# Kernel tuning notes

Measured on AMD Instinct MI355X. Metric: run time of the kernel, lower is better.

The kernel has to match this reference:

```python
import jax, jax.numpy as jnp
import numpy as np

B, S, D = 4, 2048, 768
H, DH = 12, 64  # num heads, head dim


def setup_inputs() -> dict:
    key = jax.random.key(0)
    ks = jax.random.split(key, 4)
    scale = 0.02
    return {
        "hidden_states": jax.random.normal(ks[0], (B, S, D), dtype=jnp.float32),
        "attention_mask": jnp.zeros((B, 1, 1, S), dtype=jnp.float32),
        "Wq": jax.random.normal(ks[1], (D, D), dtype=jnp.float32) * scale,
        "bq": jnp.zeros((D,), dtype=jnp.float32),
        "Wk": jax.random.normal(ks[2], (D, D), dtype=jnp.float32) * scale,
        "bk": jnp.zeros((D,), dtype=jnp.float32),
        "Wv": jax.random.normal(ks[3], (D, D), dtype=jnp.float32) * scale,
        "bv": jnp.zeros((D,), dtype=jnp.float32),
    }


def _split_heads(x):
    # [B, S, D] -> [B, H, S, DH]
    b, s, _ = x.shape
    return x.reshape(b, s, H, DH).transpose(0, 2, 1, 3)


def reference(hidden_states, attention_mask, Wq, bq, Wk, bk, Wv, bv):
    q = _split_heads(hidden_states @ Wq.T + bq)
    k = _split_heads(hidden_states @ Wk.T + bk)
    v = _split_heads(hidden_states @ Wv.T + bv)
    # scores: [B, H, S, S]
    scores = jnp.einsum("bhqd,bhkd->bhqk", q, k) / jnp.sqrt(jnp.float32(DH))
    scores = scores + attention_mask
    probs = jax.nn.softmax(scores, axis=-1)
    # dropout prob = 0.0 (eval) -> identity
    ctx = jnp.einsum("bhqk,bhkd->bhqd", probs, v)
    ctx = ctx.transpose(0, 2, 1, 3).reshape(hidden_states.shape[0], hidden_states.shape[1], D)
    return ctx
```

## Files before the change

kernel.cpp:

```cpp
#include <hip/hip_runtime.h>

#define S_LEN 2048
#define DMODEL 768
#define NH 12
#define DHEAD 64
#define BATCH 4
#define MROWS (BATCH * S_LEN)
#define NQKV 2304

using short8 = __attribute__((ext_vector_type(8))) short;
using f32x4  = __attribute__((ext_vector_type(4))) float;

typedef const __attribute__((address_space(1))) void* gas_ptr;
typedef __attribute__((address_space(3))) void* las_ptr;

__device__ __forceinline__ void gl2lds16(const void* g, void* l) {
  __builtin_amdgcn_global_load_lds((gas_ptr)(unsigned long long)g,
                                   (las_ptr)(unsigned int)(unsigned long long)l,
                                   16, 0, 0);
}

__device__ inline unsigned short f2bf(float f) {
  union { float f; unsigned int u; } c; c.f = f;
  unsigned int u = c.u;
  unsigned int r = (u + 0x7FFFu + ((u >> 16) & 1u)) >> 16;
  return (unsigned short)r;
}

__device__ inline unsigned int pack2bf(float a, float b) {
  union { float f; unsigned int u; } ca, cb;
  ca.f = a; cb.f = b;
  unsigned int ua = ca.u, ub = cb.u;
  ua = (ua + 0x7FFFu + ((ua >> 16) & 1u)) >> 16;
  ub = (ub + 0x7FFFu + ((ub >> 16) & 1u)) & 0xFFFF0000u;
  return ua | ub;
}

__global__ __launch_bounds__(256) void prep_kernel(
    const float* __restrict__ hs, const float* __restrict__ Wq,
    const float* __restrict__ Wk, const float* __restrict__ Wv,
    const float* __restrict__ mask,
    unsigned short* __restrict__ Xb, unsigned short* __restrict__ Wall,
    float* __restrict__ mask2)
{
  const int NX = MROWS * DMODEL / 4;
  const int NW = DMODEL * DMODEL / 4;
  const int NM = (BATCH * S_LEN) / 4;
  int i = blockIdx.x * 256 + threadIdx.x;
  if (i < NX) {
    float4 f = ((const float4*)hs)[i];
    ushort4 o = { f2bf(f.x), f2bf(f.y), f2bf(f.z), f2bf(f.w) };
    ((ushort4*)Xb)[i] = o;
  } else if (i < NX + 3 * NW) {
    int j = i - NX;
    int sec = j / NW, r = j - sec * NW;
    const float* src = (sec == 0) ? Wq : (sec == 1) ? Wk : Wv;
    float4 f = ((const float4*)src)[r];
    ushort4 o = { f2bf(f.x), f2bf(f.y), f2bf(f.z), f2bf(f.w) };
    ((ushort4*)(Wall + (size_t)sec * DMODEL * DMODEL))[r] = o;
  } else if (i < NX + 3 * NW + NM) {
    int r = i - NX - 3 * NW;
    float4 m = ((const float4*)mask)[r];
    float4 o = { m.x - 10.f, m.y - 10.f, m.z - 10.f, m.w - 10.f };
    ((float4*)mask2)[r] = o;
  }
}

__global__ __launch_bounds__(256) void qkv_gemm(
    const unsigned short* __restrict__ Xb,
    const unsigned short* __restrict__ Wall,
    const float* __restrict__ bq,
    const float* __restrict__ bk,
    const float* __restrict__ bv,
    unsigned short* __restrict__ Out)
{
  __shared__ __align__(16) short As[128][64];
  __shared__ __align__(16) short Bs[128][64];

  int m0 = blockIdx.y * 128;
  int n0 = blockIdx.x * 128;
  int t = threadIdx.x;
  int w = t >> 6, lane = t & 63, lg = lane >> 4, lc = lane & 15;
  int wr = (w >> 1) * 64, wc = (w & 1) * 64;

  int srow = lane >> 3;
  int schunk = (lane & 7) ^ srow;

  f32x4 acc[4][4] = {};

  for (int k0 = 0; k0 < DMODEL; k0 += 64) {
    __syncthreads();
    for (int it = 0; it < 4; ++it) {
      int rb = w * 32 + it * 8;
      int r = rb + srow;
      gl2lds16(&Xb[(size_t)(m0 + r) * DMODEL + k0 + schunk * 8], &As[rb][0]);
      gl2lds16(&Wall[(size_t)(n0 + r) * DMODEL + k0 + schunk * 8], &Bs[rb][0]);
    }
    __syncthreads();
    for (int ks = 0; ks < 2; ++ks) {
      short8 a[4], b[4];
      for (int mt = 0; mt < 4; ++mt)
        a[mt] = *(const short8*)&As[wr + mt * 16 + lc][(((ks * 4 + lg) ^ (lc & 7))) * 8];
      for (int nt = 0; nt < 4; ++nt)
        b[nt] = *(const short8*)&Bs[wc + nt * 16 + lc][(((ks * 4 + lg) ^ (lc & 7))) * 8];
      for (int mt = 0; mt < 4; ++mt)
        for (int nt = 0; nt < 4; ++nt)
          acc[mt][nt] = __builtin_amdgcn_mfma_f32_16x16x32_bf16(a[mt], b[nt], acc[mt][nt], 0, 0, 0);
    }
  }

  for (int mt = 0; mt < 4; ++mt) {
    int row = m0 + wr + mt * 16 + lg * 4;
    for (int nt = 0; nt < 4; ++nt) {
      int col = n0 + wc + nt * 16 + lc;
      float bb = (col < 768) ? bq[col] : (col < 1536) ? bk[col - 768] : bv[col - 1536];
      float sc = (col < 768) ? 0.125f : 1.0f;
      for (int i = 0; i < 4; ++i)
        Out[(size_t)(row + i) * NQKV + col] = f2bf((acc[mt][nt][i] + bb) * sc);
    }
  }
}

__global__ __launch_bounds__(256) void v_transpose(
    const unsigned short* __restrict__ QKV,
    unsigned short* __restrict__ Vt)
{
  int st = blockIdx.x, h = blockIdx.y, b = blockIdx.z;
  __shared__ __align__(16) short Ls[64][72];
  int t = threadIdx.x;
  int s0 = st * 64;
  int lr = t >> 3, ls = (t & 7) * 8;
  for (int it = 0; it < 2; ++it) {
    int r = lr + it * 32;
    *(int4*)&Ls[r][ls] =
        *(const int4*)&QKV[(size_t)(b * S_LEN + s0 + r) * NQKV + 1536 + h * DHEAD + ls];
  }
  __syncthreads();
  int d = t & 63, sq = t >> 6;
  size_t obase = ((size_t)((b * NH + h) * DHEAD + d)) * S_LEN + s0;
  for (int it = 0; it < 2; ++it) {
    int ss = sq + it * 4;
    short8 vv;
    for (int j = 0; j < 8; ++j) vv[j] = Ls[ss * 8 + j][d];
    *(short8*)&Vt[obase + ss * 8] = vv;
  }
}

__global__ __launch_bounds__(256, 6) void flash_attn(
    const unsigned short* __restrict__ QKV,
    const unsigned short* __restrict__ Vt,
    const float* __restrict__ mask2,
    float* __restrict__ out)
{
  int qt = blockIdx.x, h = blockIdx.y, b = blockIdx.z;
  __shared__ __align__(16) short Ks[64][64];
  __shared__ __align__(16) short Vts[64][64];
  __shared__ __align__(16) short Ps[4][16][72];

  int t = threadIdx.x, w = t >> 6, lane = t & 63, lg = lane >> 4, lc = lane & 15;
  int q0 = qt * 64;
  int srow = lane >> 3;
  int schunk = (lane & 7) ^ srow;

  short8 qf[2];
  {
    size_t qrow = (size_t)(b * S_LEN + q0 + w * 16 + lc) * NQKV + h * DHEAD;
    qf[0] = *(const short8*)&QKV[qrow + lg * 8];
    qf[1] = *(const short8*)&QKV[qrow + 32 + lg * 8];
  }

  f32x4 psv = {0.f, 0.f, 0.f, 0.f};
  f32x4 o[4] = {};
  size_t vtbase = (size_t)((b * NH + h) * DHEAD) * S_LEN;
  const float* mrow = mask2 + (size_t)b * S_LEN;

  for (int kt = 0; kt < S_LEN / 64; ++kt) {
    int k0 = kt * 64;
    __syncthreads();
    {
      size_t kbase = (size_t)(b * S_LEN + k0) * NQKV + 768 + h * DHEAD;
      for (int it = 0; it < 2; ++it) {
        int rb = w * 16 + it * 8;
        int r = rb + srow;
        gl2lds16(&QKV[kbase + (size_t)r * NQKV + schunk * 8], &Ks[rb][0]);
        gl2lds16(&Vt[vtbase + (size_t)r * S_LEN + k0 + schunk * 8], &Vts[rb][0]);
      }
    }
    __syncthreads();

    f32x4 s[4] = {};
    for (int kk = 0; kk < 2; ++kk)
      for (int mt = 0; mt < 4; ++mt) {
        short8 ak = *(const short8*)&Ks[mt * 16 + lc][((kk * 4 + lg) ^ (lc & 7)) * 8];
        s[mt] = __builtin_amdgcn_mfma_f32_16x16x32_bf16(ak, qf[kk], s[mt], 0, 0, 0);
      }

    for (int mt = 0; mt < 4; ++mt) {
      float4 mv = *(const float4*)&mrow[k0 + mt * 16 + lg * 4];
      float p0 = __expf(s[mt][0] + mv.x);
      float p1 = __expf(s[mt][1] + mv.y);
      float p2 = __expf(s[mt][2] + mv.z);
      float p3 = __expf(s[mt][3] + mv.w);
      psv[0] += p0; psv[1] += p1; psv[2] += p2; psv[3] += p3;
      uint2 d;
      d.x = pack2bf(p0, p1);
      d.y = pack2bf(p2, p3);
      *(uint2*)&Ps[w][lc][mt * 16 + lg * 4] = d;
    }

    __builtin_amdgcn_s_waitcnt(0);

    for (int kk = 0; kk < 2; ++kk) {
      short8 ap = *(const short8*)&Ps[w][lc][kk * 32 + lg * 8];
      for (int nt = 0; nt < 4; ++nt) {
        short8 bv = *(const short8*)&Vts[nt * 16 + lc][((kk * 4 + lg) ^ (lc & 7)) * 8];
        o[nt] = __builtin_amdgcn_mfma_f32_16x16x32_bf16(ap, bv, o[nt], 0, 0, 0);
      }
    }
  }

  float l = psv[0] + psv[1] + psv[2] + psv[3];
  l += __shfl_xor(l, 16, 64);
  l += __shfl_xor(l, 32, 64);
  float inv = 1.0f / l;
  float lv[4];
  for (int i = 0; i < 4; ++i) lv[i] = __shfl(inv, lg * 4 + i, 64);

  for (int nt = 0; nt < 4; ++nt)
    for (int i = 0; i < 4; ++i) {
      int q = q0 + w * 16 + lg * 4 + i;
      out[(size_t)(b * S_LEN + q) * DMODEL + h * DHEAD + nt * 16 + lc] = o[nt][i] * lv[i];
    }
}

extern "C" void kernel_launch(void* const* d_in, const int* in_sizes, int n_in,
                              void* d_out, int out_size, void* d_ws, size_t ws_size,
                              hipStream_t stream) {
  const float* hs   = (const float*)d_in[0];
  const float* mask = (const float*)d_in[1];
  const float* Wq   = (const float*)d_in[2];
  const float* bq   = (const float*)d_in[3];
  const float* Wk   = (const float*)d_in[4];
  const float* bk   = (const float*)d_in[5];
  const float* Wv   = (const float*)d_in[6];
  const float* bv   = (const float*)d_in[7];
  float* out = (float*)d_out;

  char* ws = (char*)d_ws;
  const size_t XB_BYTES   = (size_t)MROWS * DMODEL * 2;
  const size_t QKV_BYTES  = (size_t)MROWS * NQKV * 2;
  const size_t WALL_BYTES = (size_t)NQKV * DMODEL * 2;
  unsigned short* Xb    = (unsigned short*)ws;
  unsigned short* QKV   = (unsigned short*)(ws + XB_BYTES);
  unsigned short* Wall  = (unsigned short*)(ws + XB_BYTES + QKV_BYTES);
  float*          mask2 = (float*)(ws + XB_BYTES + QKV_BYTES + WALL_BYTES);
  unsigned short* Vtg   = Xb;

  const int NX = MROWS * DMODEL / 4;
  const int NW = DMODEL * DMODEL / 4;
  const int NM = (BATCH * S_LEN) / 4;
  int nprep = NX + 3 * NW + NM;
  prep_kernel<<<(nprep + 255) / 256, 256, 0, stream>>>(hs, Wq, Wk, Wv, mask, Xb, Wall, mask2);

  qkv_gemm<<<dim3(NQKV / 128, MROWS / 128), 256, 0, stream>>>(Xb, Wall, bq, bk, bv, QKV);

  v_transpose<<<dim3(S_LEN / 64, NH, BATCH), 256, 0, stream>>>(QKV, Vtg);

  flash_attn<<<dim3(S_LEN / 64, NH, BATCH), 256, 0, stream>>>(QKV, Vtg, mask2, out);
}
```

Measured before the change: 244.8 us.

## Switch flash attention to 32x32 MFMA with 128-row query tiles

The attention kernel now has each wave handle 32 query rows using 32x32x16 bf16 MFMA instead of 16x16x32, so each block covers 128 queries and the grid halves. Every K/V tile loaded into LDS is therefore reused across twice as many queries, which cuts global and LDS traffic per unit of work, and the larger MFMA shape needs fewer fragment loads. The cost is more registers per wave (launch bounds lowered to 4) and fewer blocks, which may reduce occupancy. The QKV GEMM epilogue loop order is also swapped so bias and scale are computed once per column.

```diff
diff --git a/kernel.cpp b/kernel.cpp
--- a/kernel.cpp
+++ b/kernel.cpp
@@ -10,6 +10,7 @@
 
 using short8 = __attribute__((ext_vector_type(8))) short;
 using f32x4  = __attribute__((ext_vector_type(4))) float;
+using f32x16 = __attribute__((ext_vector_type(16))) float;
 
 typedef const __attribute__((address_space(1))) void* gas_ptr;
 typedef __attribute__((address_space(3))) void* las_ptr;
@@ -109,12 +110,12 @@
     }
   }
 
-  for (int mt = 0; mt < 4; ++mt) {
-    int row = m0 + wr + mt * 16 + lg * 4;
-    for (int nt = 0; nt < 4; ++nt) {
-      int col = n0 + wc + nt * 16 + lc;
-      float bb = (col < 768) ? bq[col] : (col < 1536) ? bk[col - 768] : bv[col - 1536];
-      float sc = (col < 768) ? 0.125f : 1.0f;
+  for (int nt = 0; nt < 4; ++nt) {
+    int col = n0 + wc + nt * 16 + lc;
+    float bb = (col < 768) ? bq[col] : (col < 1536) ? bk[col - 768] : bv[col - 1536];
+    float sc = (col < 768) ? 0.125f : 1.0f;
+    for (int mt = 0; mt < 4; ++mt) {
+      int row = m0 + wr + mt * 16 + lg * 4;
       for (int i = 0; i < 4; ++i)
         Out[(size_t)(row + i) * NQKV + col] = f2bf((acc[mt][nt][i] + bb) * sc);
     }
@@ -146,7 +147,7 @@
   }
 }
 
-__global__ __launch_bounds__(256, 6) void flash_attn(
+__global__ __launch_bounds__(256, 4) void flash_attn(
     const unsigned short* __restrict__ QKV,
     const unsigned short* __restrict__ Vt,
     const float* __restrict__ mask2,
@@ -155,22 +156,23 @@
   int qt = blockIdx.x, h = blockIdx.y, b = blockIdx.z;
   __shared__ __align__(16) short Ks[64][64];
   __shared__ __align__(16) short Vts[64][64];
-  __shared__ __align__(16) short Ps[4][16][72];
-
-  int t = threadIdx.x, w = t >> 6, lane = t & 63, lg = lane >> 4, lc = lane & 15;
-  int q0 = qt * 64;
+  __shared__ __align__(16) short Ps[4][32][68];
+
+  int t = threadIdx.x, w = t >> 6, lane = t & 63;
+  int m31 = lane & 31, hf = lane >> 5;
+  int q0 = qt * 128;
   int srow = lane >> 3;
   int schunk = (lane & 7) ^ srow;
 
-  short8 qf[2];
+  short8 qf[4];
   {
-    size_t qrow = (size_t)(b * S_LEN + q0 + w * 16 + lc) * NQKV + h * DHEAD;
-    qf[0] = *(const short8*)&QKV[qrow + lg * 8];
-    qf[1] = *(const short8*)&QKV[qrow + 32 + lg * 8];
-  }
-
-  f32x4 psv = {0.f, 0.f, 0.f, 0.f};
-  f32x4 o[4] = {};
+    size_t qrow = (size_t)(b * S_LEN + q0 + w * 32 + m31) * NQKV + h * DHEAD;
+    for (int kk = 0; kk < 4; ++kk)
+      qf[kk] = *(const short8*)&QKV[qrow + kk * 16 + hf * 8];
+  }
+
+  float lsum = 0.f;
+  f32x16 o[2] = {};
   size_t vtbase = (size_t)((b * NH + h) * DHEAD) * S_LEN;
   const float* mrow = mask2 + (size_t)b * S_LEN;
 
@@ -188,48 +190,51 @@
     }
     __syncthreads();
 
-    f32x4 s[4] = {};
-    for (int kk = 0; kk < 2; ++kk)
-      for (int mt = 0; mt < 4; ++mt) {
-        short8 ak = *(const short8*)&Ks[mt * 16 + lc][((kk * 4 + lg) ^ (lc & 7)) * 8];
-        s[mt] = __builtin_amdgcn_mfma_f32_16x16x32_bf16(ak, qf[kk], s[mt], 0, 0, 0);
-      }
-
-    for (int mt = 0; mt < 4; ++mt) {
-      float4 mv = *(const float4*)&mrow[k0 + mt * 16 + lg * 4];
-      float p0 = __expf(s[mt][0] + mv.x);
-      float p1 = __expf(s[mt][1] + mv.y);
-      float p2 = __expf(s[mt][2] + mv.z);
-      float p3 = __expf(s[mt][3] + mv.w);
-      psv[0] += p0; psv[1] += p1; psv[2] += p2; psv[3] += p3;
-      uint2 d;
-      d.x = pack2bf(p0, p1);
-      d.y = pack2bf(p2, p3);
-      *(uint2*)&Ps[w][lc][mt * 16 + lg * 4] = d;
-    }
+    f32x16 s[2] = {};
+    for (int kk = 0; kk < 4; ++kk)
+      for (int mt = 0; mt < 2; ++mt) {
+        int r = mt * 32 + m31;
+        short8 ak = *(const short8*)&Ks[r][((kk * 2 + hf) ^ (r & 7)) * 8];
+        s[mt] = __builtin_amdgcn_mfma_f32_32x32x16_bf16(ak, qf[kk], s[mt], 0, 0, 0);
+      }
+
+    for (int mt = 0; mt < 2; ++mt)
+      for (int g = 0; g < 4; ++g) {
+        float4 mv = *(const float4*)&mrow[k0 + mt * 32 + g * 8 + hf * 4];
+        float p0 = __expf(s[mt][g * 4 + 0] + mv.x);
+        float p1 = __expf(s[mt][g * 4 + 1] + mv.y);
+        float p2 = __expf(s[mt][g * 4 + 2] + mv.z);
+        float p3 = __expf(s[mt][g * 4 + 3] + mv.w);
+        lsum += (p0 + p1) + (p2 + p3);
+        uint2 d2;
+        d2.x = pack2bf(p0, p1);
+        d2.y = pack2bf(p2, p3);
+        *(uint2*)&Ps[w][m31][mt * 32 + g * 8 + hf * 4] = d2;
+      }
 
     __builtin_amdgcn_s_waitcnt(0);
 
-    for (int kk = 0; kk < 2; ++kk) {
-      short8 ap = *(const short8*)&Ps[w][lc][kk * 32 + lg * 8];
-      for (int nt = 0; nt < 4; ++nt) {
-        short8 bv = *(const short8*)&Vts[nt * 16 + lc][((kk * 4 + lg) ^ (lc & 7)) * 8];
-        o[nt] = __builtin_amdgcn_mfma_f32_16x16x32_bf16(ap, bv, o[nt], 0, 0, 0);
-      }
-    }
-  }
-
-  float l = psv[0] + psv[1] + psv[2] + psv[3];
-  l += __shfl_xor(l, 16, 64);
-  l += __shfl_xor(l, 32, 64);
-  float inv = 1.0f / l;
-  float lv[4];
-  for (int i = 0; i < 4; ++i) lv[i] = __shfl(inv, lg * 4 + i, 64);
-
-  for (int nt = 0; nt < 4; ++nt)
-    for (int i = 0; i < 4; ++i) {
-      int q = q0 + w * 16 + lg * 4 + i;
-      out[(size_t)(b * S_LEN + q) * DMODEL + h * DHEAD + nt * 16 + lc] = o[nt][i] * lv[i];
+    for (int kk = 0; kk < 4; ++kk) {
+      short8 ap = *(const short8*)&Ps[w][m31][kk * 16 + hf * 8];
+      for (int nt = 0; nt < 2; ++nt) {
+        int r = nt * 32 + m31;
+        short8 bv = *(const short8*)&Vts[r][((kk * 2 + hf) ^ (r & 7)) * 8];
+        o[nt] = __builtin_amdgcn_mfma_f32_32x32x16_bf16(ap, bv, o[nt], 0, 0, 0);
+      }
+    }
+  }
+
+  lsum += __shfl_xor(lsum, 32, 64);
+  float inv = 1.0f / lsum;
+  float lv[16];
+  for (int r = 0; r < 16; ++r)
+    lv[r] = __shfl(inv, (r & 3) + 8 * (r >> 2) + 4 * hf, 64);
+
+  for (int nt = 0; nt < 2; ++nt)
+    for (int r = 0; r < 16; ++r) {
+      int qrow = (r & 3) + 8 * (r >> 2) + 4 * hf;
+      int q = q0 + w * 32 + qrow;
+      out[(size_t)(b * S_LEN + q) * DMODEL + h * DHEAD + nt * 32 + m31] = o[nt][r] * lv[r];
     }
 }
 
@@ -266,5 +271,5 @@
 
   v_transpose<<<dim3(S_LEN / 64, NH, BATCH), 256, 0, stream>>>(QKV, Vtg);
 
-  flash_attn<<<dim3(S_LEN / 64, NH, BATCH), 256, 0, stream>>>(QKV, Vtg, mask2, out);
-}
+  flash_attn<<<dim3(S_LEN / 128, NH, BATCH), 256, 0, stream>>>(QKV, Vtg, mask2, out);
+}
```

After: 236.2 us. 1.04x faster.
